# Optimization experiments

Measured on AMD Instinct MI355X. Metric: run time of the kernel, lower is better.

Reference implementation:

```python
import jax, jax.numpy as jnp
import numpy as np

N_POINTS = 500_000
N_WAVES = 128


def setup_inputs() -> dict:
    key = jax.random.key(0)
    k1, k2, k3, k4 = jax.random.split(key, 4)
    x = jax.random.uniform(k1, (N_POINTS, 2), dtype=jnp.float32)  # 2D coords in [0,1)
    # wavelengths ~ U(0,3) -> freqs = 1/wavelength (as in add_next_wave)
    freqs = 1.0 / (3.0 * jax.random.uniform(k2, (N_WAVES, 1), dtype=jnp.float32) + 1e-2)
    rotations = jnp.pi * jax.random.uniform(k3, (N_WAVES, 1), dtype=jnp.float32)
    coeffs = jax.random.normal(k4, (N_WAVES, 2), dtype=jnp.float32)
    return {"x": x, "freqs": freqs, "rotations": rotations, "coeffs": coeffs}


def reference(x, freqs, rotations, coeffs):
    # x: [N,2]; freqs, rotations: [W,1]; coeffs: [W,2]
    two_pi = 2.0 * jnp.pi
    # rotated coordinate along each wave's direction: [N,W,1]
    rotated_x = (x[:, None, 0:1] * jnp.cos(rotations)[None, :]
                 + x[:, None, 1:2] * jnp.sin(rotations)[None, :])
    phase = two_pi * rotated_x * freqs[None, :]  # [N,W,1]
    vals = (coeffs[None, :, 0:1] * jnp.sin(phase)
            + coeffs[None, :, 1:2] * jnp.cos(phase))  # [N,W,1]
    return jnp.sum(vals, axis=1)  # [N,1]
```

## Files before the change

kernel.cpp:

```cpp
#include <hip/hip_runtime.h>
#include <math.h>

#define N_WAVES 128
#define BLOCK 256
#define PPT 2


__global__ __launch_bounds__(BLOCK) void periodic2d_kernel(
    const float* __restrict__ x,
    const float* __restrict__ freqs,
    const float* __restrict__ rots,
    const float* __restrict__ coeffs,
    float* __restrict__ out,
    int n)
{
    __shared__ float4 wp[N_WAVES];

    const int tid = threadIdx.x;
    if (tid < N_WAVES) {
        float f  = freqs[tid];
        float r  = rots[tid];
        float c0 = coeffs[2 * tid];
        float c1 = coeffs[2 * tid + 1];
        float sr, cr;
        sincosf(r, &sr, &cr);
        float amp = sqrtf(c0 * c0 + c1 * c1);
        float phi = atan2f(c1, c0) * 0.15915494309189535f;
        wp[tid] = make_float4(f * cr, f * sr, phi, amp);
    }
    __syncthreads();

    const int ia = blockIdx.x * (BLOCK * PPT) + tid;
    const int ib = ia + BLOCK;

    const float2* __restrict__ X2 = (const float2*)x;
    float x0a = 0.f, x1a = 0.f, x0b = 0.f, x1b = 0.f;
    if (ia < n) { float2 v = X2[ia]; x0a = v.x; x1a = v.y; }
    if (ib < n) { float2 v = X2[ib]; x0b = v.x; x1b = v.y; }

    float acca = 0.f, accb = 0.f;
#pragma unroll 8
    for (int w = 0; w < N_WAVES; ++w) {
        float4 p = wp[w];
        float pa = __builtin_fmaf(p.x, x0a, __builtin_fmaf(p.y, x1a, p.z));
        float ta = __builtin_amdgcn_fractf(pa);
        float sa = __builtin_amdgcn_sinf(ta);
        acca = __builtin_fmaf(p.w, sa, acca);
        float pb = __builtin_fmaf(p.x, x0b, __builtin_fmaf(p.y, x1b, p.z));
        float tb = __builtin_amdgcn_fractf(pb);
        float sb = __builtin_amdgcn_sinf(tb);
        accb = __builtin_fmaf(p.w, sb, accb);
    }

    if (ia < n) out[ia] = acca;
    if (ib < n) out[ib] = accb;
}

extern "C" void kernel_launch(void* const* d_in, const int* in_sizes, int n_in,
                              void* d_out, int out_size, void* d_ws, size_t ws_size,
                              hipStream_t stream) {
    const float* x      = (const float*)d_in[0];
    const float* freqs  = (const float*)d_in[1];
    const float* rots   = (const float*)d_in[2];
    const float* coeffs = (const float*)d_in[3];
    float* out = (float*)d_out;

    const int n = out_size;
    const int grid = (n + BLOCK * PPT - 1) / (BLOCK * PPT);
    periodic2d_kernel<<<grid, BLOCK, 0, stream>>>(x, freqs, rots, coeffs, out, n);
}
```

Before: 71.11 us.

## Precompute wave parameters in a setup kernel and process four points per thread

Moves the per-block sincos/atan2/sqrt computation of wave parameters into a separate one-block setup kernel that writes to workspace, so each main block only copies 128 float4 values into shared memory. Points per thread go from 2 to 4 and the inner loop is generalised to an array of accumulators, so each LDS parameter load is reused across more points. The cost is an extra kernel launch with a serial dependency, and fewer blocks (about 489 for 500k points) on a GPU with many CUs, which may underfill the device.

```diff
diff --git a/kernel.cpp b/kernel.cpp
--- a/kernel.cpp
+++ b/kernel.cpp
@@ -3,57 +3,67 @@
 
 #define N_WAVES 128
 #define BLOCK 256
-#define PPT 2
+#define PPT 4
 
+
+__global__ void setup_kernel(const float* __restrict__ freqs,
+                             const float* __restrict__ rots,
+                             const float* __restrict__ coeffs,
+                             float4* __restrict__ wp_out) {
+    int w = threadIdx.x;
+    if (w < N_WAVES) {
+        float f  = freqs[w];
+        float r  = rots[w];
+        float c0 = coeffs[2 * w];
+        float c1 = coeffs[2 * w + 1];
+        float sr, cr;
+        sincosf(r, &sr, &cr);
+        float amp = sqrtf(c0 * c0 + c1 * c1);
+        float phi = atan2f(c1, c0) * 0.15915494309189535f;
+        wp_out[w] = make_float4(f * cr, f * sr, phi, amp);
+    }
+}
 
 __global__ __launch_bounds__(BLOCK) void periodic2d_kernel(
     const float* __restrict__ x,
-    const float* __restrict__ freqs,
-    const float* __restrict__ rots,
-    const float* __restrict__ coeffs,
+    const float4* __restrict__ wp_g,
     float* __restrict__ out,
     int n)
 {
     __shared__ float4 wp[N_WAVES];
-
     const int tid = threadIdx.x;
-    if (tid < N_WAVES) {
-        float f  = freqs[tid];
-        float r  = rots[tid];
-        float c0 = coeffs[2 * tid];
-        float c1 = coeffs[2 * tid + 1];
-        float sr, cr;
-        sincosf(r, &sr, &cr);
-        float amp = sqrtf(c0 * c0 + c1 * c1);
-        float phi = atan2f(c1, c0) * 0.15915494309189535f;
-        wp[tid] = make_float4(f * cr, f * sr, phi, amp);
-    }
+    if (tid < N_WAVES) wp[tid] = wp_g[tid];
     __syncthreads();
 
-    const int ia = blockIdx.x * (BLOCK * PPT) + tid;
-    const int ib = ia + BLOCK;
+    const float2* __restrict__ X2 = (const float2*)x;
+    const int base = blockIdx.x * (BLOCK * PPT) + tid;
 
-    const float2* __restrict__ X2 = (const float2*)x;
-    float x0a = 0.f, x1a = 0.f, x0b = 0.f, x1b = 0.f;
-    if (ia < n) { float2 v = X2[ia]; x0a = v.x; x1a = v.y; }
-    if (ib < n) { float2 v = X2[ib]; x0b = v.x; x1b = v.y; }
+    float x0[PPT], x1[PPT], acc[PPT];
+#pragma unroll
+    for (int k = 0; k < PPT; ++k) {
+        int i = base + k * BLOCK;
+        x0[k] = 0.f; x1[k] = 0.f; acc[k] = 0.f;
+        if (i < n) { float2 v = X2[i]; x0[k] = v.x; x1[k] = v.y; }
+    }
 
-    float acca = 0.f, accb = 0.f;
-#pragma unroll 8
+#pragma unroll 4
     for (int w = 0; w < N_WAVES; ++w) {
         float4 p = wp[w];
-        float pa = __builtin_fmaf(p.x, x0a, __builtin_fmaf(p.y, x1a, p.z));
-        float ta = __builtin_amdgcn_fractf(pa);
-        float sa = __builtin_amdgcn_sinf(ta);
-        acca = __builtin_fmaf(p.w, sa, acca);
-        float pb = __builtin_fmaf(p.x, x0b, __builtin_fmaf(p.y, x1b, p.z));
-        float tb = __builtin_amdgcn_fractf(pb);
-        float sb = __builtin_amdgcn_sinf(tb);
-        accb = __builtin_fmaf(p.w, sb, accb);
+#pragma unroll
+        for (int k = 0; k < PPT; ++k) {
+            float ph = __builtin_fmaf(p.x, x0[k],
+                        __builtin_fmaf(p.y, x1[k], p.z));
+            float t  = __builtin_amdgcn_fractf(ph);
+            float s  = __builtin_amdgcn_sinf(t);
+            acc[k]   = __builtin_fmaf(p.w, s, acc[k]);
+        }
     }
 
-    if (ia < n) out[ia] = acca;
-    if (ib < n) out[ib] = accb;
+#pragma unroll
+    for (int k = 0; k < PPT; ++k) {
+        int i = base + k * BLOCK;
+        if (i < n) out[i] = acc[k];
+    }
 }
 
 extern "C" void kernel_launch(void* const* d_in, const int* in_sizes, int n_in,
@@ -64,8 +74,10 @@
     const float* rots   = (const float*)d_in[2];
     const float* coeffs = (const float*)d_in[3];
     float* out = (float*)d_out;
+    float4* wp = (float4*)d_ws;
 
     const int n = out_size;
+    setup_kernel<<<1, N_WAVES, 0, stream>>>(freqs, rots, coeffs, wp);
     const int grid = (n + BLOCK * PPT - 1) / (BLOCK * PPT);
-    periodic2d_kernel<<<grid, BLOCK, 0, stream>>>(x, freqs, rots, coeffs, out, n);
+    periodic2d_kernel<<<grid, BLOCK, 0, stream>>>(x, wp, out, n);
 }
```

Result: slower. 73.37 us (+3.2%).
